# Kernel tuning notes

Hardware: AMD Instinct MI355X
Metric: run time of the kernel (lower is better)

The kernel has to match this reference:

```python
import jax, jax.numpy as jnp
import numpy as np

B, T, IN, H, GAT_HEADS, MHA_HEADS, C = 32, 512, 128, 256, 4, 4, 8
OUT = H // GAT_HEADS          # 64, GAT per-head out_features
HD = H // MHA_HEADS           # 64, MHA head dim
ALPHA = 0.2                   # LeakyReLU slope
EPS = 1e-5                    # LayerNorm eps


def setup_inputs() -> dict:
    key = jax.random.key(0)
    ks = iter(jax.random.split(key, 32))
    def rn(shape, scale=0.05):
        return jax.random.normal(next(ks), shape, dtype=jnp.float32) * scale
    return {
        "x": jax.random.normal(next(ks), (B, T, IN), dtype=jnp.float32),
        # GRU layer 0 / 1 (PyTorch gate order r,z,n)
        "gru_W_ih0": rn((3 * H, IN)), "gru_W_hh0": rn((3 * H, H)),
        "gru_b_ih0": rn((3 * H,)), "gru_b_hh0": rn((3 * H,)),
        "gru_W_ih1": rn((3 * H, H)), "gru_W_hh1": rn((3 * H, H)),
        "gru_b_ih1": rn((3 * H,)), "gru_b_hh1": rn((3 * H,)),
        # GAT: per-head W [H,OUT] and additive attention vector a [2*OUT]
        "gat_W": rn((GAT_HEADS, H, OUT)), "gat_a": rn((GAT_HEADS, 2 * OUT)),
        "ln_g": jnp.ones((H,), jnp.float32), "ln_b": jnp.zeros((H,), jnp.float32),
        # MHA packed in-proj (q,k,v) + out-proj
        "mha_in_w": rn((3 * H, H)), "mha_in_b": rn((3 * H,)),
        "mha_out_w": rn((H, H)), "mha_out_b": rn((H,)),
        "fc1_w": rn((H // 2, H)), "fc1_b": rn((H // 2,)),
        "fc2_w": rn((C, H // 2)), "fc2_b": rn((C,)),
    }


def _gru_layer(x, W_ih, W_hh, b_ih, b_hh):
    # x: [B,T,D] -> hidden states [B,T,H]; PyTorch GRU cell math, gates r,z,n
    xp = jnp.einsum('btd,gd->btg', x, W_ih) + b_ih  # precompute input proj [B,T,3H]
    Hh = W_hh.shape[1]
    def step(h, xp_t):
        g = h @ W_hh.T + b_hh
        xr, xz, xn = jnp.split(xp_t, 3, axis=-1)
        hr, hz, hn = jnp.split(g, 3, axis=-1)
        r = jax.nn.sigmoid(xr + hr)
        z = jax.nn.sigmoid(xz + hz)
        n = jnp.tanh(xn + r * hn)
        h_new = (1.0 - z) * n + z * h
        return h_new, h_new
    h0 = jnp.zeros((x.shape[0], Hh), x.dtype)
    _, hs = jax.lax.scan(step, h0, jnp.swapaxes(xp, 0, 1))
    return jnp.swapaxes(hs, 0, 1)


def _gat_head(h_in, W, a):
    # Additive attention decomposed: e_ij = leakyrelu(a1.h_i + a2.h_j)
    # (exactly equals matmul(cat[h_i,h_j], a) without the [B,T,T,2*OUT] tensor)
    h = h_in @ W                       # [B,T,OUT]
    f_src = h @ a[:OUT]                # [B,T]
    f_dst = h @ a[OUT:]                # [B,T]
    e = jax.nn.leaky_relu(f_src[:, :, None] + f_dst[:, None, :], ALPHA)  # [B,T,T]
    attn = jax.nn.softmax(e, axis=-1)  # dropout is identity in eval mode
    return jnp.einsum('bij,bjd->bid', attn, h)


def _layer_norm(x, g, b):
    mu = x.mean(-1, keepdims=True)
    var = jnp.mean((x - mu) ** 2, -1, keepdims=True)
    return (x - mu) * jax.lax.rsqrt(var + EPS) * g + b


def _forward(x, gru_W_ih0, gru_W_hh0, gru_b_ih0, gru_b_hh0,
             gru_W_ih1, gru_W_hh1, gru_b_ih1, gru_b_hh1,
             gat_W, gat_a, ln_g, ln_b,
             mha_in_w, mha_in_b, mha_out_w, mha_out_b,
             fc1_w, fc1_b, fc2_w, fc2_b):
    g = _gru_layer(x, gru_W_ih0, gru_W_hh0, gru_b_ih0, gru_b_hh0)
    g = _gru_layer(g, gru_W_ih1, gru_W_hh1, gru_b_ih1, gru_b_hh1)  # [B,T,H]
    gat_out = jnp.concatenate([_gat_head(g, gat_W[i], gat_a[i]) for i in range(GAT_HEADS)], axis=-1)
    y = _layer_norm(g + gat_out, ln_g, ln_b)
    # Multihead self-attention (4 heads, eval-mode dropout = identity)
    qkv = y @ mha_in_w.T + mha_in_b
    q, k, v = jnp.split(qkv, 3, axis=-1)
    def split_heads(t):
        return t.reshape(t.shape[0], t.shape[1], MHA_HEADS, HD).transpose(0, 2, 1, 3)
    q, k, v = split_heads(q), split_heads(k), split_heads(v)
    scores = jnp.einsum('bhqd,bhkd->bhqk', q, k) / jnp.sqrt(jnp.float32(HD))
    attn = jax.nn.softmax(scores, axis=-1)
    ctx = jnp.einsum('bhqk,bhkd->bhqd', attn, v)
    ctx = ctx.transpose(0, 2, 1, 3).reshape(y.shape[0], y.shape[1], H)
    attn_out = ctx @ mha_out_w.T + mha_out_b
    pooled = attn_out.mean(axis=1)                    # [B,H]
    hid = jax.nn.relu(pooled @ fc1_w.T + fc1_b)
    return hid @ fc2_w.T + fc2_b                      # [B,C]


def reference(x, gru_W_ih0, gru_W_hh0, gru_b_ih0, gru_b_hh0,
              gru_W_ih1, gru_W_hh1, gru_b_ih1, gru_b_hh1,
              gat_W, gat_a, ln_g, ln_b,
              mha_in_w, mha_in_b, mha_out_w, mha_out_b,
              fc1_w, fc1_b, fc2_w, fc2_b):
    return _forward(x, gru_W_ih0, gru_W_hh0, gru_b_ih0, gru_b_hh0,
                    gru_W_ih1, gru_W_hh1, gru_b_ih1, gru_b_hh1,
                    gat_W, gat_a, ln_g, ln_b,
                    mha_in_w, mha_in_b, mha_out_w, mha_out_b,
                    fc1_w, fc1_b, fc2_w, fc2_b)
```

## Files before the change

kernel.cpp:

```cpp
#include <hip/hip_runtime.h>
#include <math.h>

#define BB 32
#define TT 512
#define INF_ 128
#define HH 256
#define H3 768
#define NHEADS 4
#define HDIM 64

typedef _Float16 half_t;
typedef half_t half2_t __attribute__((ext_vector_type(2)));
typedef half_t half4_t __attribute__((ext_vector_type(4)));
typedef half_t f16x8 __attribute__((ext_vector_type(8)));
typedef float f32x4 __attribute__((ext_vector_type(4)));

#if defined(__has_builtin)
#if __has_builtin(__builtin_amdgcn_fdot2)
#define FDOT2(a, b, c) __builtin_amdgcn_fdot2((a), (b), (c), false)
#endif
#endif
#ifndef FDOT2
#define FDOT2(a, b, c) fmaf((float)(a).x, (float)(b).x, fmaf((float)(a).y, (float)(b).y, (c)))
#endif

#define BCH(x) __builtin_bit_cast(half2_t, x)
#define PKH(a, b) __builtin_bit_cast(unsigned, half2_t{(half_t)(a), (half_t)(b)})

__device__ __forceinline__ float wsum(float v) {
#pragma unroll
  for (int o = 32; o > 0; o >>= 1) v += __shfl_xor(v, o, 64);
  return v;
}
__device__ __forceinline__ float wmax(float v) {
#pragma unroll
  for (int o = 32; o > 0; o >>= 1) v = fmaxf(v, __shfl_xor(v, o, 64));
  return v;
}

__global__ void castk(const float* __restrict__ s, half_t* __restrict__ d, int n) {
  int i = (blockIdx.x * 256 + threadIdx.x) * 4;
  if (i < n) {
    float4 v = *(const float4*)(s + i);
    half4_t o = {(half_t)v.x, (half_t)v.y, (half_t)v.z, (half_t)v.w};
    *(half4_t*)(d + i) = o;
  }
}

__device__ __forceinline__ f16x8 pk16(float4 a, float4 b) {
  return f16x8{(half_t)a.x, (half_t)a.y, (half_t)a.z, (half_t)a.w,
               (half_t)b.x, (half_t)b.y, (half_t)b.z, (half_t)b.w};
}

__global__ __launch_bounds__(256) void gemm_f16(
    const half_t* __restrict__ A, const half_t* __restrict__ B,
    const float* __restrict__ bias, float* __restrict__ C,
    int M, int N, int K) {
  __shared__ __align__(16) half_t As[128][40];
  __shared__ __align__(16) half_t Bs[64][40];
  const int tid = threadIdx.x;
  const int wave = tid >> 6, lane = tid & 63;
  const int m0 = blockIdx.y * 128, n0 = blockIdx.x * 64;
  const int mrow = lane & 15, quad = lane >> 4;
  f32x4 acc00 = {0.f, 0.f, 0.f, 0.f}, acc01 = acc00, acc02 = acc00, acc03 = acc00;
  f32x4 acc10 = acc00, acc11 = acc00, acc12 = acc00, acc13 = acc00;
  for (int k0 = 0; k0 < K; k0 += 32) {
    __syncthreads();
#pragma unroll
    for (int u = 0; u < 2; ++u) {
      int idx = tid + u * 256;
      int row = idx >> 2, seg = idx & 3;
      *(f16x8*)&As[row][seg * 8] =
          *(const f16x8*)&A[(size_t)(m0 + row) * K + k0 + seg * 8];
    }
    {
      int row = tid >> 2, seg = tid & 3;
      *(f16x8*)&Bs[row][seg * 8] =
          *(const f16x8*)&B[(size_t)(n0 + row) * K + k0 + seg * 8];
    }
    __syncthreads();
    f16x8 af0 = *(const f16x8*)&As[wave * 32 + mrow][quad * 8];
    f16x8 af1 = *(const f16x8*)&As[wave * 32 + 16 + mrow][quad * 8];
    f16x8 bf0 = *(const f16x8*)&Bs[mrow][quad * 8];
    f16x8 bf1 = *(const f16x8*)&Bs[16 + mrow][quad * 8];
    f16x8 bf2 = *(const f16x8*)&Bs[32 + mrow][quad * 8];
    f16x8 bf3 = *(const f16x8*)&Bs[48 + mrow][quad * 8];
    acc00 = __builtin_amdgcn_mfma_f32_16x16x32_f16(af0, bf0, acc00, 0, 0, 0);
    acc01 = __builtin_amdgcn_mfma_f32_16x16x32_f16(af0, bf1, acc01, 0, 0, 0);
    acc02 = __builtin_amdgcn_mfma_f32_16x16x32_f16(af0, bf2, acc02, 0, 0, 0);
    acc03 = __builtin_amdgcn_mfma_f32_16x16x32_f16(af0, bf3, acc03, 0, 0, 0);
    acc10 = __builtin_amdgcn_mfma_f32_16x16x32_f16(af1, bf0, acc10, 0, 0, 0);
    acc11 = __builtin_amdgcn_mfma_f32_16x16x32_f16(af1, bf1, acc11, 0, 0, 0);
    acc12 = __builtin_amdgcn_mfma_f32_16x16x32_f16(af1, bf2, acc12, 0, 0, 0);
    acc13 = __builtin_amdgcn_mfma_f32_16x16x32_f16(af1, bf3, acc13, 0, 0, 0);
  }
  float bv0 = bias ? bias[n0 + mrow] : 0.f;
  float bv1 = bias ? bias[n0 + 16 + mrow] : 0.f;
  float bv2 = bias ? bias[n0 + 32 + mrow] : 0.f;
  float bv3 = bias ? bias[n0 + 48 + mrow] : 0.f;
  const int rb = m0 + wave * 32 + quad * 4;
#pragma unroll
  for (int r = 0; r < 4; ++r) {
    float* c0 = C + (size_t)(rb + r) * N + n0;
    c0[mrow] = acc00[r] + bv0;
    c0[16 + mrow] = acc01[r] + bv1;
    c0[32 + mrow] = acc02[r] + bv2;
    c0[48 + mrow] = acc03[r] + bv3;
    float* c1 = C + (size_t)(rb + 16 + r) * N + n0;
    c1[mrow] = acc10[r] + bv0;
    c1[16 + mrow] = acc11[r] + bv1;
    c1[32 + mrow] = acc12[r] + bv2;
    c1[48 + mrow] = acc13[r] + bv3;
  }
}

#define LDW(g, p, a, b, i)                             \
  {                                                    \
    float4 v = (p)[i];                                 \
    g##a = half2_t{(half_t)v.x, (half_t)v.y};          \
    g##b = half2_t{(half_t)v.z, (half_t)v.w};          \
  }
#define LDW32(g, p)                                                        \
  LDW(g, p, 0, 1, 0) LDW(g, p, 2, 3, 1) LDW(g, p, 4, 5, 2)                 \
  LDW(g, p, 6, 7, 3) LDW(g, p, 8, 9, 4) LDW(g, p, 10, 11, 5)               \
  LDW(g, p, 12, 13, 6) LDW(g, p, 14, 15, 7) LDW(g, p, 16, 17, 8)           \
  LDW(g, p, 18, 19, 9) LDW(g, p, 20, 21, 10) LDW(g, p, 22, 23, 11)         \
  LDW(g, p, 24, 25, 12) LDW(g, p, 26, 27, 13) LDW(g, p, 28, 29, 14)        \
  LDW(g, p, 30, 31, 15) LDW(g, p, 32, 33, 16) LDW(g, p, 34, 35, 17)        \
  LDW(g, p, 36, 37, 18) LDW(g, p, 38, 39, 19) LDW(g, p, 40, 41, 20)        \
  LDW(g, p, 42, 43, 21) LDW(g, p, 44, 45, 22) LDW(g, p, 46, 47, 23)        \
  LDW(g, p, 48, 49, 24) LDW(g, p, 50, 51, 25) LDW(g, p, 52, 53, 26)        \
  LDW(g, p, 54, 55, 27) LDW(g, p, 56, 57, 28) LDW(g, p, 58, 59, 29)        \
  LDW(g, p, 60, 61, 30) LDW(g, p, 62, 63, 31)

#define DECL64(g)                                                          \
  half2_t g##0, g##1, g##2, g##3, g##4, g##5, g##6, g##7, g##8, g##9,      \
      g##10, g##11, g##12, g##13, g##14, g##15, g##16, g##17, g##18,       \
      g##19, g##20, g##21, g##22, g##23, g##24, g##25, g##26, g##27,       \
      g##28, g##29, g##30, g##31, g##32, g##33, g##34, g##35, g##36,       \
      g##37, g##38, g##39, g##40, g##41, g##42, g##43, g##44, g##45,       \
      g##46, g##47, g##48, g##49, g##50, g##51, g##52, g##53, g##54,       \
      g##55, g##56, g##57, g##58, g##59, g##60, g##61, g##62, g##63;

#define CHR(c8, a0, a1, a2, a3)                                            \
  {                                                                        \
    float4 v = hp4[c8];                                                    \
    half2_t t0 = __builtin_bit_cast(half2_t, v.x);                         \
    half2_t t1 = __builtin_bit_cast(half2_t, v.y);                         \
    half2_t t2 = __builtin_bit_cast(half2_t, v.z);                         \
    half2_t t3 = __builtin_bit_cast(half2_t, v.w);                         \
    ar = FDOT2(wr##a0, t0, ar); az = FDOT2(wz##a0, t0, az); an = FDOT2(wn##a0, t0, an); \
    ar = FDOT2(wr##a1, t1, ar); az = FDOT2(wz##a1, t1, az); an = FDOT2(wn##a1, t1, an); \
    ar = FDOT2(wr##a2, t2, ar); az = FDOT2(wz##a2, t2, az); an = FDOT2(wn##a2, t2, an); \
    ar = FDOT2(wr##a3, t3, ar); az = FDOT2(wz##a3, t3, az); an = FDOT2(wn##a3, t3, an); \
  }

__global__ __launch_bounds__(512, 2) void gru_layer(
    const float* __restrict__ xp, const float* __restrict__ Whh,
    const float* __restrict__ bhh, float* __restrict__ out,
    half_t* __restrict__ out16) {
  __shared__ __align__(16) half_t hs[2][2][144];
  const int tid = threadIdx.x;
  const int kh = tid & 1, j = tid >> 1;
  const int b = blockIdx.x;
  const bool wf32 = (out != nullptr);
  DECL64(wr)
  DECL64(wz)
  DECL64(wn)
  {
    const float4* pr = (const float4*)(Whh + (size_t)j * HH + kh * 128);
    const float4* pz = (const float4*)(Whh + (size_t)(HH + j) * HH + kh * 128);
    const float4* pn = (const float4*)(Whh + (size_t)(2 * HH + j) * HH + kh * 128);
    LDW32(wr, pr)
    LDW32(wz, pz)
    LDW32(wn, pn)
  }
  const float br = bhh[j], bz = bhh[HH + j], bn = bhh[2 * HH + j];
  for (int i = tid; i < 288; i += 512) ((unsigned*)hs)[i] = 0u;
  __syncthreads();
  float hprev = 0.f;
  const float* xrow = xp + (size_t)b * TT * H3;
  float* orow = out + (size_t)b * TT * HH;
  half_t* orow16 = out16 + (size_t)b * TT * HH;
  for (int t = 0; t < TT; ++t) {
    float xr = xrow[j], xz = xrow[HH + j], xn = xrow[2 * HH + j];
    const float4* hp4 = (const float4*)&hs[t & 1][kh][0];
    float ar = 0.f, az = 0.f, an = 0.f;
    CHR(0, 0, 1, 2, 3)
    CHR(1, 4, 5, 6, 7)
    CHR(2, 8, 9, 10, 11)
    CHR(3, 12, 13, 14, 15)
    CHR(4, 16, 17, 18, 19)
    CHR(5, 20, 21, 22, 23)
    CHR(6, 24, 25, 26, 27)
    CHR(7, 28, 29, 30, 31)
    CHR(8, 32, 33, 34, 35)
    CHR(9, 36, 37, 38, 39)
    CHR(10, 40, 41, 42, 43)
    CHR(11, 44, 45, 46, 47)
    CHR(12, 48, 49, 50, 51)
    CHR(13, 52, 53, 54, 55)
    CHR(14, 56, 57, 58, 59)
    CHR(15, 60, 61, 62, 63)
    ar += __shfl_xor(ar, 1);
    az += __shfl_xor(az, 1);
    an += __shfl_xor(an, 1);
    float rg = 1.f / (1.f + __expf(-(xr + ar + br)));
    float zg = 1.f / (1.f + __expf(-(xz + az + bz)));
    float ng = 2.f / (1.f + __expf(-2.f * (xn + rg * (an + bn)))) - 1.f;
    float hnew = (1.f - zg) * ng + zg * hprev;
    hprev = hnew;
    float hpart = __shfl_xor(hnew, 2);
    if ((tid & 3) == 0) {
      half2_t pk;
      pk.x = (half_t)hnew;
      pk.y = (half_t)hpart;
      *(half2_t*)&hs[(t + 1) & 1][j >> 7][j & 127] = pk;
    }
    if (kh == 0) {
      orow16[j] = (half_t)hnew;
      if (wf32) orow[j] = hnew;
    }
    __syncthreads();
    xrow += H3;
    orow += HH;
    orow16 += HH;
  }
}

__global__ void gat_wt(const float* __restrict__ W, half_t* __restrict__ Wt) {
  int idx = blockIdx.x * 256 + threadIdx.x;
  int col = idx >> 8, k = idx & 255;
  Wt[idx] = (half_t)W[((size_t)((col >> 6) * HH + k)) * HDIM + (col & 63)];
}

__global__ void gat_fsd(const float* __restrict__ hgat, const float* __restrict__ a,
                        float* __restrict__ fsrc, float* __restrict__ fdst) {
  int b = blockIdx.x, hd = blockIdx.y, t = threadIdx.x;
  const float* hp = hgat + ((size_t)(b * TT + t)) * HH + hd * HDIM;
  const float* ap = a + hd * 2 * HDIM;
  float fs = 0.f, fd = 0.f;
#pragma unroll 4
  for (int d = 0; d < HDIM; ++d) {
    float hv = hp[d];
    fs += hv * ap[d];
    fd += hv * ap[HDIM + d];
  }
  fsrc[(b * NHEADS + hd) * TT + t] = fs;
  fdst[(b * NHEADS + hd) * TT + t] = fd;
}

__global__ __launch_bounds__(256) void gat_attn(
    const float* __restrict__ hgat, const float* __restrict__ fsrc,
    const float* __restrict__ fdst, float* __restrict__ out) {
  __shared__ __align__(16) half_t Htt[64][136];
  __shared__ __align__(16) half_t Ps[4][16][136];
  __shared__ __align__(16) float fd[128];
  const int tid = threadIdx.x, wave = tid >> 6, lane = tid & 63;
  const int mrow = lane & 15, quad = lane >> 4;
  const int hd = blockIdx.y, b = blockIdx.z;
  const int q0 = blockIdx.x * 64;
  const float fi = fsrc[(size_t)(b * NHEADS + hd) * TT + q0 + wave * 16 + mrow];
  const float* fdp = fdst + (size_t)(b * NHEADS + hd) * TT;
  float m = -1e30f, l = 0.f;
  f32x4 o[4];
#pragma unroll
  for (int n = 0; n < 4; ++n) o[n] = f32x4{0.f, 0.f, 0.f, 0.f};
  for (int jt = 0; jt < TT; jt += 128) {
#pragma unroll
    for (int u = 0; u < 4; ++u) {
      int idx = tid + u * 256;
      int j = idx >> 3, s = (idx & 7) * 8;
      const float* hp = hgat + (size_t)(b * TT + jt + j) * HH + hd * HDIM + s;
      float4 ha = *(const float4*)hp, hb = *(const float4*)(hp + 4);
      Htt[s + 0][j] = (half_t)ha.x; Htt[s + 1][j] = (half_t)ha.y;
      Htt[s + 2][j] = (half_t)ha.z; Htt[s + 3][j] = (half_t)ha.w;
      Htt[s + 4][j] = (half_t)hb.x; Htt[s + 5][j] = (half_t)hb.y;
      Htt[s + 6][j] = (half_t)hb.z; Htt[s + 7][j] = (half_t)hb.w;
    }
    if (tid < 32) *(float4*)&fd[tid * 4] = *(const float4*)&fdp[jt + tid * 4];
    __syncthreads();
    float p[32];
    float mx = -1e30f;
#pragma unroll
    for (int g = 0; g < 8; ++g) {
      float4 f4 = *(const float4*)&fd[quad * 32 + g * 4];
      float e0 = fi + f4.x; e0 = (e0 > 0.f) ? e0 : 0.2f * e0;
      float e1 = fi + f4.y; e1 = (e1 > 0.f) ? e1 : 0.2f * e1;
      float e2 = fi + f4.z; e2 = (e2 > 0.f) ? e2 : 0.2f * e2;
      float e3 = fi + f4.w; e3 = (e3 > 0.f) ? e3 : 0.2f * e3;
      p[g * 4 + 0] = e0; p[g * 4 + 1] = e1; p[g * 4 + 2] = e2; p[g * 4 + 3] = e3;
      mx = fmaxf(mx, fmaxf(fmaxf(e0, e1), fmaxf(e2, e3)));
    }
    mx = fmaxf(mx, __shfl_xor(mx, 16, 64));
    mx = fmaxf(mx, __shfl_xor(mx, 32, 64));
    float mn = fmaxf(m, mx);
    float corr = __expf(m - mn);
    m = mn;
    float ls = 0.f;
#pragma unroll
    for (int i = 0; i < 32; ++i) { p[i] = __expf(p[i] - mn); ls += p[i]; }
    ls += __shfl_xor(ls, 16, 64);
    ls += __shfl_xor(ls, 32, 64);
    l = l * corr + ls;
    float cr[4];
#pragma unroll
    for (int r = 0; r < 4; ++r) cr[r] = __shfl(corr, quad * 4 + r, 64);
#pragma unroll
    for (int n = 0; n < 4; ++n) {
      o[n][0] *= cr[0]; o[n][1] *= cr[1]; o[n][2] *= cr[2]; o[n][3] *= cr[3];
    }
#pragma unroll
    for (int s8 = 0; s8 < 4; ++s8) {
      f16x8 pkv = {(half_t)p[s8 * 8 + 0], (half_t)p[s8 * 8 + 1],
                   (half_t)p[s8 * 8 + 2], (half_t)p[s8 * 8 + 3],
                   (half_t)p[s8 * 8 + 4], (half_t)p[s8 * 8 + 5],
                   (half_t)p[s8 * 8 + 6], (half_t)p[s8 * 8 + 7]};
      *(f16x8*)&Ps[wave][mrow][quad * 32 + s8 * 8] = pkv;
    }
    __syncthreads();
    f16x8 pa0 = *(const f16x8*)&Ps[wave][mrow][0 * 32 + quad * 8];
    f16x8 pa1 = *(const f16x8*)&Ps[wave][mrow][1 * 32 + quad * 8];
    f16x8 pa2 = *(const f16x8*)&Ps[wave][mrow][2 * 32 + quad * 8];
    f16x8 pa3 = *(const f16x8*)&Ps[wave][mrow][3 * 32 + quad * 8];
#pragma unroll
    for (int n = 0; n < 4; ++n) {
      f16x8 vb0 = *(const f16x8*)&Htt[n * 16 + mrow][0 * 32 + quad * 8];
      f16x8 vb1 = *(const f16x8*)&Htt[n * 16 + mrow][1 * 32 + quad * 8];
      f16x8 vb2 = *(const f16x8*)&Htt[n * 16 + mrow][2 * 32 + quad * 8];
      f16x8 vb3 = *(const f16x8*)&Htt[n * 16 + mrow][3 * 32 + quad * 8];
      o[n] = __builtin_amdgcn_mfma_f32_16x16x32_f16(pa0, vb0, o[n], 0, 0, 0);
      o[n] = __builtin_amdgcn_mfma_f32_16x16x32_f16(pa1, vb1, o[n], 0, 0, 0);
      o[n] = __builtin_amdgcn_mfma_f32_16x16x32_f16(pa2, vb2, o[n], 0, 0, 0);
      o[n] = __builtin_amdgcn_mfma_f32_16x16x32_f16(pa3, vb3, o[n], 0, 0, 0);
    }
    __syncthreads();
  }
  float lr[4];
#pragma unroll
  for (int r = 0; r < 4; ++r) lr[r] = __shfl(l, quad * 4 + r, 64);
#pragma unroll
  for (int n = 0; n < 4; ++n)
#pragma unroll
    for (int r = 0; r < 4; ++r)
      out[(size_t)(b * TT + q0 + wave * 16 + quad * 4 + r) * HH + hd * HDIM +
          n * 16 + mrow] = o[n][r] / lr[r];
}

__global__ __launch_bounds__(256) void ln_res(
    const float* __restrict__ g, const float* __restrict__ gat,
    const float* __restrict__ gamma, const float* __restrict__ beta,
    half_t* __restrict__ y16) {
  int wave = threadIdx.x >> 6, lane = threadIdx.x & 63;
  size_t n = (size_t)blockIdx.x * 4 + wave;
  float4 v = ((const float4*)(g + n * HH))[lane];
  float4 w = ((const float4*)(gat + n * HH))[lane];
  v.x += w.x; v.y += w.y; v.z += w.z; v.w += w.w;
  float mu = wsum(v.x + v.y + v.z + v.w) * (1.f / 256.f);
  float dx = v.x - mu, dy = v.y - mu, dz = v.z - mu, dw = v.w - mu;
  float var = wsum(dx * dx + dy * dy + dz * dz + dw * dw) * (1.f / 256.f);
  float rstd = rsqrtf(var + 1e-5f);
  float4 gm = ((const float4*)gamma)[lane];
  float4 bt = ((const float4*)beta)[lane];
  half4_t o = {(half_t)(dx * rstd * gm.x + bt.x), (half_t)(dy * rstd * gm.y + bt.y),
               (half_t)(dz * rstd * gm.z + bt.z), (half_t)(dw * rstd * gm.w + bt.w)};
  ((half4_t*)(y16 + n * HH))[lane] = o;
}

__global__ __launch_bounds__(256) void mha_attn(const float* __restrict__ qkv,
                                                half_t* __restrict__ ctx16) {
  __shared__ __align__(16) half_t Qs[64][72];
  __shared__ __align__(16) half_t Ks[128][72];
  __shared__ __align__(16) half_t Vt[64][136];
  __shared__ __align__(16) half_t Ps[4][16][136];
  const int tid = threadIdx.x, wave = tid >> 6, lane = tid & 63;
  const int mrow = lane & 15, quad = lane >> 4;
  const int hd = blockIdx.y, b = blockIdx.z;
  const int q0 = blockIdx.x * 64;
  {
    int r = tid >> 2, s = (tid & 3) * 16;
    const float* src = qkv + (size_t)(b * TT + q0 + r) * H3 + hd * HDIM + s;
    float4 a = *(const float4*)src, b4 = *(const float4*)(src + 4);
    float4 c = *(const float4*)(src + 8), d4 = *(const float4*)(src + 12);
    *(f16x8*)&Qs[r][s] = pk16(a, b4);
    *(f16x8*)&Qs[r][s + 8] = pk16(c, d4);
  }
  __syncthreads();
  f16x8 qa0 = *(const f16x8*)&Qs[wave * 16 + mrow][quad * 8];
  f16x8 qa1 = *(const f16x8*)&Qs[wave * 16 + mrow][32 + quad * 8];
  float m[4] = {-1e30f, -1e30f, -1e30f, -1e30f};
  float l[4] = {0.f, 0.f, 0.f, 0.f};
  f32x4 o[4];
#pragma unroll
  for (int n = 0; n < 4; ++n) o[n] = f32x4{0.f, 0.f, 0.f, 0.f};
  for (int jt = 0; jt < TT; jt += 128) {
#pragma unroll
    for (int u = 0; u < 4; ++u) {
      int idx = tid + u * 256;
      int j = idx >> 3, s = (idx & 7) * 8;
      const float* kp = qkv + (size_t)(b * TT + jt + j) * H3 + HH + hd * HDIM + s;
      float4 ka = *(const float4*)kp, kb = *(const float4*)(kp + 4);
      *(f16x8*)&Ks[j][s] = pk16(ka, kb);
      const float* vp = kp + HH;
      float4 va = *(const float4*)vp, vb = *(const float4*)(vp + 4);
      Vt[s + 0][j] = (half_t)va.x; Vt[s + 1][j] = (half_t)va.y;
      Vt[s + 2][j] = (half_t)va.z; Vt[s + 3][j] = (half_t)va.w;
      Vt[s + 4][j] = (half_t)vb.x; Vt[s + 5][j] = (half_t)vb.y;
      Vt[s + 6][j] = (half_t)vb.z; Vt[s + 7][j] = (half_t)vb.w;
    }
    __syncthreads();
    f32x4 sAcc[8];
#pragma unroll
    for (int n = 0; n < 8; ++n) sAcc[n] = f32x4{0.f, 0.f, 0.f, 0.f};
#pragma unroll
    for (int n = 0; n < 8; ++n) {
      f16x8 kb0 = *(const f16x8*)&Ks[n * 16 + mrow][quad * 8];
      f16x8 kb1 = *(const f16x8*)&Ks[n * 16 + mrow][32 + quad * 8];
      sAcc[n] = __builtin_amdgcn_mfma_f32_16x16x32_f16(qa0, kb0, sAcc[n], 0, 0, 0);
      sAcc[n] = __builtin_amdgcn_mfma_f32_16x16x32_f16(qa1, kb1, sAcc[n], 0, 0, 0);
    }
    float p[8][4];
    float mx[4] = {-1e30f, -1e30f, -1e30f, -1e30f};
#pragma unroll
    for (int n = 0; n < 8; ++n)
#pragma unroll
      for (int r = 0; r < 4; ++r) {
        float v = sAcc[n][r] * 0.125f;
        p[n][r] = v;
        mx[r] = fmaxf(mx[r], v);
      }
#pragma unroll
    for (int off = 8; off > 0; off >>= 1)
#pragma unroll
      for (int r = 0; r < 4; ++r) mx[r] = fmaxf(mx[r], __shfl_xor(mx[r], off, 64));
    float corr[4], ls[4];
#pragma unroll
    for (int r = 0; r < 4; ++r) {
      float mn = fmaxf(m[r], mx[r]);
      corr[r] = __expf(m[r] - mn);
      m[r] = mn;
      ls[r] = 0.f;
    }
#pragma unroll
    for (int n = 0; n < 8; ++n)
#pragma unroll
      for (int r = 0; r < 4; ++r) {
        float e = __expf(p[n][r] - m[r]);
        p[n][r] = e;
        ls[r] += e;
      }
#pragma unroll
    for (int off = 8; off > 0; off >>= 1)
#pragma unroll
      for (int r = 0; r < 4; ++r) ls[r] += __shfl_xor(ls[r], off, 64);
#pragma unroll
    for (int r = 0; r < 4; ++r) l[r] = l[r] * corr[r] + ls[r];
#pragma unroll
    for (int n = 0; n < 4; ++n) {
      o[n][0] *= corr[0]; o[n][1] *= corr[1]; o[n][2] *= corr[2]; o[n][3] *= corr[3];
    }
#pragma unroll
    for (int n = 0; n < 8; ++n)
#pragma unroll
      for (int r = 0; r < 4; ++r)
        Ps[wave][quad * 4 + r][n * 16 + mrow] = (half_t)p[n][r];
    __syncthreads();
    f16x8 pa0 = *(const f16x8*)&Ps[wave][mrow][0 * 32 + quad * 8];
    f16x8 pa1 = *(const f16x8*)&Ps[wave][mrow][1 * 32 + quad * 8];
    f16x8 pa2 = *(const f16x8*)&Ps[wave][mrow][2 * 32 + quad * 8];
    f16x8 pa3 = *(const f16x8*)&Ps[wave][mrow][3 * 32 + quad * 8];
#pragma unroll
    for (int n = 0; n < 4; ++n) {
      f16x8 vb0 = *(const f16x8*)&Vt[n * 16 + mrow][0 * 32 + quad * 8];
      f16x8 vb1 = *(const f16x8*)&Vt[n * 16 + mrow][1 * 32 + quad * 8];
      f16x8 vb2 = *(const f16x8*)&Vt[n * 16 + mrow][2 * 32 + quad * 8];
      f16x8 vb3 = *(const f16x8*)&Vt[n * 16 + mrow][3 * 32 + quad * 8];
      o[n] = __builtin_amdgcn_mfma_f32_16x16x32_f16(pa0, vb0, o[n], 0, 0, 0);
      o[n] = __builtin_amdgcn_mfma_f32_16x16x32_f16(pa1, vb1, o[n], 0, 0, 0);
      o[n] = __builtin_amdgcn_mfma_f32_16x16x32_f16(pa2, vb2, o[n], 0, 0, 0);
      o[n] = __builtin_amdgcn_mfma_f32_16x16x32_f16(pa3, vb3, o[n], 0, 0, 0);
    }
    __syncthreads();
  }
#pragma unroll
  for (int n = 0; n < 4; ++n)
#pragma unroll
    for (int r = 0; r < 4; ++r)
      ctx16[(size_t)(b * TT + q0 + wave * 16 + quad * 4 + r) * HH + hd * HDIM +
            n * 16 + mrow] = (half_t)(o[n][r] / l[r]);
}

__global__ void mean_pool(const float* __restrict__ x, float* __restrict__ out) {
  int b = blockIdx.x, j = threadIdx.x;
  const float* p = x + (size_t)b * TT * HH + j;
  float s = 0.f;
  for (int t = 0; t < TT; ++t) s += p[(size_t)t * HH];
  out[b * HH + j] = s * (1.f / 512.f);
}

__global__ void fc1_k(const float* __restrict__ pooled, const float* __restrict__ w,
                      const float* __restrict__ bias, float* __restrict__ hid) {
  int b = blockIdx.x, o = threadIdx.x;
  const float* pp = pooled + b * HH;
  const float* wp = w + o * HH;
  float s = 0.f;
#pragma unroll 4
  for (int k = 0; k < HH; ++k) s += pp[k] * wp[k];
  hid[b * 128 + o] = fmaxf(s + bias[o], 0.f);
}

__global__ void fc2_k(const float* __restrict__ hid, const float* __restrict__ w,
                      const float* __restrict__ bias, float* __restrict__ out) {
  int t = threadIdx.x;
  int mm = t >> 3, c = t & 7;
  const float* hp = hid + mm * 128;
  const float* wp = w + c * 128;
  float s = 0.f;
#pragma unroll 4
  for (int k = 0; k < 128; ++k) s += hp[k] * wp[k];
  out[mm * 8 + c] = s + bias[c];
}

extern "C" void kernel_launch(void* const* d_in, const int* in_sizes, int n_in,
                              void* d_out, int out_size, void* d_ws, size_t ws_size,
                              hipStream_t stream) {
  (void)in_sizes; (void)n_in; (void)out_size; (void)ws_size;
  const float* x    = (const float*)d_in[0];
  const float* Wih0 = (const float*)d_in[1];
  const float* Whh0 = (const float*)d_in[2];
  const float* bih0 = (const float*)d_in[3];
  const float* bhh0 = (const float*)d_in[4];
  const float* Wih1 = (const float*)d_in[5];
  const float* Whh1 = (const float*)d_in[6];
  const float* bih1 = (const float*)d_in[7];
  const float* bhh1 = (const float*)d_in[8];
  const float* gatW = (const float*)d_in[9];
  const float* gatA = (const float*)d_in[10];
  const float* lng  = (const float*)d_in[11];
  const float* lnb  = (const float*)d_in[12];
  const float* inw  = (const float*)d_in[13];
  const float* inb  = (const float*)d_in[14];
  const float* outw = (const float*)d_in[15];
  const float* outb = (const float*)d_in[16];
  const float* f1w  = (const float*)d_in[17];
  const float* f1b  = (const float*)d_in[18];
  const float* f2w  = (const float*)d_in[19];
  const float* f2b  = (const float*)d_in[20];
  float* out = (float*)d_out;
  float* ws = (float*)d_ws;

  float* XPA   = ws;
  float* G0    = ws + 12582912;
  float* G1    = G0 + 4194304;
  float* Yb    = G1 + 4194304;
  float* HGAT  = Yb + 4194304;
  float* GATWTf= HGAT + 4194304;
  float* FSRC  = GATWTf + 65536;
  float* FDST  = FSRC + 65536;
  float* POOL  = FDST + 65536;
  float* HIDb  = POOL + 8192;
  float* W16b  = HIDb + 4096;

  half_t* X16     = (half_t*)G1;
  half_t* G0_16   = (half_t*)Yb;
  half_t* G1_16   = (half_t*)(Yb + 2097152);
  half_t* CTX16   = (half_t*)HGAT;
  half_t* Y16     = (half_t*)(HGAT + 2097152);
  half_t* GATWT16 = (half_t*)GATWTf;
  half_t* W16ih0  = (half_t*)W16b;
  half_t* W16ih1  = (half_t*)(W16b + 49152);
  half_t* W16in   = (half_t*)(W16b + 49152 + 98304);
  half_t* W16out  = (half_t*)(W16b + 49152 + 98304 + 98304);

  castk<<<2048, 256, 0, stream>>>(x, X16, 2097152);
  castk<<<96, 256, 0, stream>>>(Wih0, W16ih0, 98304);
  castk<<<192, 256, 0, stream>>>(Wih1, W16ih1, 196608);
  castk<<<192, 256, 0, stream>>>(inw, W16in, 196608);
  castk<<<64, 256, 0, stream>>>(outw, W16out, 65536);
  gat_wt<<<256, 256, 0, stream>>>(gatW, GATWT16);
  gemm_f16<<<dim3(12, 128), 256, 0, stream>>>(X16, W16ih0, bih0, XPA, 16384, 768, 128);
  gru_layer<<<32, 512, 0, stream>>>(XPA, Whh0, bhh0, nullptr, G0_16);
  gemm_f16<<<dim3(12, 128), 256, 0, stream>>>(G0_16, W16ih1, bih1, XPA, 16384, 768, 256);
  gru_layer<<<32, 512, 0, stream>>>(XPA, Whh1, bhh1, G1, G1_16);
  gemm_f16<<<dim3(4, 128), 256, 0, stream>>>(G1_16, GATWT16, nullptr, HGAT, 16384, 256, 256);
  gat_fsd<<<dim3(32, 4), 512, 0, stream>>>(HGAT, gatA, FSRC, FDST);
  gat_attn<<<dim3(8, 4, 32), 256, 0, stream>>>(HGAT, FSRC, FDST, G0);
  ln_res<<<4096, 256, 0, stream>>>(G1, G0, lng, lnb, Y16);
  gemm_f16<<<dim3(12, 128), 256, 0, stream>>>(Y16, W16in, inb, XPA, 16384, 768, 256);
  mha_attn<<<dim3(8, 4, 32), 256, 0, stream>>>(XPA, CTX16);
  gemm_f16<<<dim3(4, 128), 256, 0, stream>>>(CTX16, W16out, outb, Yb, 16384, 256, 256);
  mean_pool<<<32, 256, 0, stream>>>(Yb, POOL);
  fc1_k<<<32, 128, 0, stream>>>(POOL, f1w, f1b, HIDb);
  fc2_k<<<1, 256, 0, stream>>>(HIDb, f2w, f2b, out);
}
```

Baseline: 1.641 ms.

## Split GRU recurrent dot products four ways across 1024-thread blocks

The GRU recurrence kernel now assigns four threads per hidden unit instead of two. Each thread holds a quarter of the W_hh rows in registers and reduces with two xor shuffles. The shared hidden-state buffer layout changes to four 64-element slices, and each hidden value is written directly by one thread instead of being packed in pairs. This halves the serial dot-product chain per timestep and the register footprint per thread, at the cost of an extra shuffle stage and a barrier across more waves per step.

```diff
diff --git a/kernel.cpp b/kernel.cpp
--- a/kernel.cpp
+++ b/kernel.cpp
@@ -25,7 +25,6 @@
 #endif
 
 #define BCH(x) __builtin_bit_cast(half2_t, x)
-#define PKH(a, b) __builtin_bit_cast(unsigned, half2_t{(half_t)(a), (half_t)(b)})
 
 __device__ __forceinline__ float wsum(float v) {
 #pragma unroll
@@ -120,63 +119,52 @@
     g##a = half2_t{(half_t)v.x, (half_t)v.y};          \
     g##b = half2_t{(half_t)v.z, (half_t)v.w};          \
   }
-#define LDW32(g, p)                                                        \
+#define LDW16(g, p)                                                        \
   LDW(g, p, 0, 1, 0) LDW(g, p, 2, 3, 1) LDW(g, p, 4, 5, 2)                 \
   LDW(g, p, 6, 7, 3) LDW(g, p, 8, 9, 4) LDW(g, p, 10, 11, 5)               \
   LDW(g, p, 12, 13, 6) LDW(g, p, 14, 15, 7) LDW(g, p, 16, 17, 8)           \
   LDW(g, p, 18, 19, 9) LDW(g, p, 20, 21, 10) LDW(g, p, 22, 23, 11)         \
   LDW(g, p, 24, 25, 12) LDW(g, p, 26, 27, 13) LDW(g, p, 28, 29, 14)        \
-  LDW(g, p, 30, 31, 15) LDW(g, p, 32, 33, 16) LDW(g, p, 34, 35, 17)        \
-  LDW(g, p, 36, 37, 18) LDW(g, p, 38, 39, 19) LDW(g, p, 40, 41, 20)        \
-  LDW(g, p, 42, 43, 21) LDW(g, p, 44, 45, 22) LDW(g, p, 46, 47, 23)        \
-  LDW(g, p, 48, 49, 24) LDW(g, p, 50, 51, 25) LDW(g, p, 52, 53, 26)        \
-  LDW(g, p, 54, 55, 27) LDW(g, p, 56, 57, 28) LDW(g, p, 58, 59, 29)        \
-  LDW(g, p, 60, 61, 30) LDW(g, p, 62, 63, 31)
-
-#define DECL64(g)                                                          \
+  LDW(g, p, 30, 31, 15)
+
+#define DECL32(g)                                                          \
   half2_t g##0, g##1, g##2, g##3, g##4, g##5, g##6, g##7, g##8, g##9,      \
       g##10, g##11, g##12, g##13, g##14, g##15, g##16, g##17, g##18,       \
       g##19, g##20, g##21, g##22, g##23, g##24, g##25, g##26, g##27,       \
-      g##28, g##29, g##30, g##31, g##32, g##33, g##34, g##35, g##36,       \
-      g##37, g##38, g##39, g##40, g##41, g##42, g##43, g##44, g##45,       \
-      g##46, g##47, g##48, g##49, g##50, g##51, g##52, g##53, g##54,       \
-      g##55, g##56, g##57, g##58, g##59, g##60, g##61, g##62, g##63;
-
-#define CHR(c8, a0, a1, a2, a3)                                            \
+      g##28, g##29, g##30, g##31;
+
+#define CH4(c, a0, a1, a2, a3)                                             \
   {                                                                        \
-    float4 v = hp4[c8];                                                    \
-    half2_t t0 = __builtin_bit_cast(half2_t, v.x);                         \
-    half2_t t1 = __builtin_bit_cast(half2_t, v.y);                         \
-    half2_t t2 = __builtin_bit_cast(half2_t, v.z);                         \
-    half2_t t3 = __builtin_bit_cast(half2_t, v.w);                         \
+    float4 v = hp4[c];                                                     \
+    half2_t t0 = BCH(v.x), t1 = BCH(v.y), t2 = BCH(v.z), t3 = BCH(v.w);    \
     ar = FDOT2(wr##a0, t0, ar); az = FDOT2(wz##a0, t0, az); an = FDOT2(wn##a0, t0, an); \
     ar = FDOT2(wr##a1, t1, ar); az = FDOT2(wz##a1, t1, az); an = FDOT2(wn##a1, t1, an); \
     ar = FDOT2(wr##a2, t2, ar); az = FDOT2(wz##a2, t2, az); an = FDOT2(wn##a2, t2, an); \
     ar = FDOT2(wr##a3, t3, ar); az = FDOT2(wz##a3, t3, az); an = FDOT2(wn##a3, t3, an); \
   }
 
-__global__ __launch_bounds__(512, 2) void gru_layer(
+__global__ __launch_bounds__(1024, 4) void gru_layer(
     const float* __restrict__ xp, const float* __restrict__ Whh,
     const float* __restrict__ bhh, float* __restrict__ out,
     half_t* __restrict__ out16) {
-  __shared__ __align__(16) half_t hs[2][2][144];
+  __shared__ __align__(16) half_t hs[2][4][72];
   const int tid = threadIdx.x;
-  const int kh = tid & 1, j = tid >> 1;
+  const int kh = tid & 3, j = tid >> 2;
   const int b = blockIdx.x;
   const bool wf32 = (out != nullptr);
-  DECL64(wr)
-  DECL64(wz)
-  DECL64(wn)
+  DECL32(wr)
+  DECL32(wz)
+  DECL32(wn)
   {
-    const float4* pr = (const float4*)(Whh + (size_t)j * HH + kh * 128);
-    const float4* pz = (const float4*)(Whh + (size_t)(HH + j) * HH + kh * 128);
-    const float4* pn = (const float4*)(Whh + (size_t)(2 * HH + j) * HH + kh * 128);
-    LDW32(wr, pr)
-    LDW32(wz, pz)
-    LDW32(wn, pn)
+    const float4* pr = (const float4*)(Whh + (size_t)j * HH + kh * 64);
+    const float4* pz = (const float4*)(Whh + (size_t)(HH + j) * HH + kh * 64);
+    const float4* pn = (const float4*)(Whh + (size_t)(2 * HH + j) * HH + kh * 64);
+    LDW16(wr, pr)
+    LDW16(wz, pz)
+    LDW16(wn, pn)
   }
   const float br = bhh[j], bz = bhh[HH + j], bn = bhh[2 * HH + j];
-  for (int i = tid; i < 288; i += 512) ((unsigned*)hs)[i] = 0u;
+  for (int i = tid; i < 288; i += 1024) ((unsigned*)hs)[i] = 0u;
   __syncthreads();
   float hprev = 0.f;
   const float* xrow = xp + (size_t)b * TT * H3;
@@ -186,38 +174,24 @@
     float xr = xrow[j], xz = xrow[HH + j], xn = xrow[2 * HH + j];
     const float4* hp4 = (const float4*)&hs[t & 1][kh][0];
     float ar = 0.f, az = 0.f, an = 0.f;
-    CHR(0, 0, 1, 2, 3)
-    CHR(1, 4, 5, 6, 7)
-    CHR(2, 8, 9, 10, 11)
-    CHR(3, 12, 13, 14, 15)
-    CHR(4, 16, 17, 18, 19)
-    CHR(5, 20, 21, 22, 23)
-    CHR(6, 24, 25, 26, 27)
-    CHR(7, 28, 29, 30, 31)
-    CHR(8, 32, 33, 34, 35)
-    CHR(9, 36, 37, 38, 39)
-    CHR(10, 40, 41, 42, 43)
-    CHR(11, 44, 45, 46, 47)
-    CHR(12, 48, 49, 50, 51)
-    CHR(13, 52, 53, 54, 55)
-    CHR(14, 56, 57, 58, 59)
-    CHR(15, 60, 61, 62, 63)
-    ar += __shfl_xor(ar, 1);
-    az += __shfl_xor(az, 1);
-    an += __shfl_xor(an, 1);
+    CH4(0, 0, 1, 2, 3)
+    CH4(1, 4, 5, 6, 7)
+    CH4(2, 8, 9, 10, 11)
+    CH4(3, 12, 13, 14, 15)
+    CH4(4, 16, 17, 18, 19)
+    CH4(5, 20, 21, 22, 23)
+    CH4(6, 24, 25, 26, 27)
+    CH4(7, 28, 29, 30, 31)
+    ar += __shfl_xor(ar, 1); ar += __shfl_xor(ar, 2);
+    az += __shfl_xor(az, 1); az += __shfl_xor(az, 2);
+    an += __shfl_xor(an, 1); an += __shfl_xor(an, 2);
     float rg = 1.f / (1.f + __expf(-(xr + ar + br)));
     float zg = 1.f / (1.f + __expf(-(xz + az + bz)));
     float ng = 2.f / (1.f + __expf(-2.f * (xn + rg * (an + bn)))) - 1.f;
     float hnew = (1.f - zg) * ng + zg * hprev;
     hprev = hnew;
-    float hpart = __shfl_xor(hnew, 2);
-    if ((tid & 3) == 0) {
-      half2_t pk;
-      pk.x = (half_t)hnew;
-      pk.y = (half_t)hpart;
-      *(half2_t*)&hs[(t + 1) & 1][j >> 7][j & 127] = pk;
-    }
     if (kh == 0) {
+      hs[(t + 1) & 1][j >> 6][j & 63] = (half_t)hnew;
       orow16[j] = (half_t)hnew;
       if (wf32) orow[j] = hnew;
     }
@@ -579,9 +553,9 @@
   castk<<<64, 256, 0, stream>>>(outw, W16out, 65536);
   gat_wt<<<256, 256, 0, stream>>>(gatW, GATWT16);
   gemm_f16<<<dim3(12, 128), 256, 0, stream>>>(X16, W16ih0, bih0, XPA, 16384, 768, 128);
-  gru_layer<<<32, 512, 0, stream>>>(XPA, Whh0, bhh0, nullptr, G0_16);
+  gru_layer<<<32, 1024, 0, stream>>>(XPA, Whh0, bhh0, nullptr, G0_16);
   gemm_f16<<<dim3(12, 128), 256, 0, stream>>>(G0_16, W16ih1, bih1, XPA, 16384, 768, 256);
-  gru_layer<<<32, 512, 0, stream>>>(XPA, Whh1, bhh1, G1, G1_16);
+  gru_layer<<<32, 1024, 0, stream>>>(XPA, Whh1, bhh1, G1, G1_16);
   gemm_f16<<<dim3(4, 128), 256, 0, stream>>>(G1_16, GATWT16, nullptr, HGAT, 16384, 256, 256);
   gat_fsd<<<dim3(32, 4), 512, 0, stream>>>(HGAT, gatA, FSRC, FDST);
   gat_attn<<<dim3(8, 4, 32), 256, 0, stream>>>(HGAT, FSRC, FDST, G0);
```

After: 1.848 ms. +12.6%, slower.
